# Performance work log

Measured on AMD Instinct MI355X. Metric: run time of the kernel, lower is better.

## Reference

```python
import jax, jax.numpy as jnp
import numpy as np

B, S, E, H = 4, 2048, 1024, 16
D = E // H  # head_dim


def setup_inputs() -> dict:
    key = jax.random.key(0)
    ks = jax.random.split(key, 6)
    x = jax.random.normal(ks[0], (B, S, E), dtype=jnp.float32)
    # causal mask: 1 where attention allowed (lower triangular)
    mask = jnp.tril(jnp.ones((S, S), dtype=bool))
    scale = 1.0 / jnp.sqrt(E).astype(jnp.float32)  # init scale for linears
    w_q = jax.random.normal(ks[1], (E, E), dtype=jnp.float32) * scale
    w_k = jax.random.normal(ks[2], (E, E), dtype=jnp.float32) * scale
    w_v = jax.random.normal(ks[3], (E, E), dtype=jnp.float32) * scale
    w_o = jax.random.normal(ks[4], (E, E), dtype=jnp.float32) * scale
    b_o = jnp.zeros((E,), dtype=jnp.float32)
    return {"x": x, "mask": mask, "w_q": w_q, "w_k": w_k, "w_v": w_v,
            "w_o": w_o, "b_o": b_o}


def reference(x, mask, w_q, w_k, w_v, w_o, b_o):
    # torch Linear: y = x @ W.T ; weights stored [out, in]
    q = jnp.einsum('bse,fe->bsf', x, w_q).reshape(B, S, H, D).transpose(0, 2, 1, 3)
    k = jnp.einsum('bse,fe->bsf', x, w_k).reshape(B, S, H, D).transpose(0, 2, 1, 3)
    v = jnp.einsum('bse,fe->bsf', x, w_v).reshape(B, S, H, D).transpose(0, 2, 1, 3)
    scale = D ** -0.5
    scores = jnp.einsum('bhqd,bhkd->bhqk', q, k) * scale  # [B,H,S,S]
    scores = jnp.where(mask, scores, -jnp.inf)
    attn = jax.nn.softmax(scores, axis=-1)
    out = jnp.einsum('bhqk,bhkd->bhqd', attn, v)  # [B,H,S,D]
    out = out.transpose(0, 2, 1, 3).reshape(B, S, E)
    return jnp.einsum('bse,fe->bsf', out, w_o) + b_o
```

## Files before the change

kernel.cpp:

```cpp
#include <hip/hip_runtime.h>
#include <stdint.h>

#define B_ 4
#define S_ 2048
#define E_ 1024
#define H_ 16
#define D_ 64
#define LSTR 72
#define PSTR 72

typedef __bf16 bf16x8 __attribute__((ext_vector_type(8)));
typedef float f32x4 __attribute__((ext_vector_type(4)));

__device__ __forceinline__ f32x4 mfma16(bf16x8 a, bf16x8 b, f32x4 c) {
    return __builtin_amdgcn_mfma_f32_16x16x32_bf16(a, b, c, 0, 0, 0);
}

__device__ __forceinline__ float expsm(float s) {
    const float x = __builtin_fmaf(s, 0.18033688f, -17.31234049f);
    float r;
    asm("v_exp_f32 %0, %1" : "=v"(r) : "v"(x));
    return r;
}

__device__ __forceinline__ bf16x8 cvt8(const float* p) {
    const f32x4 a = *(const f32x4*)p;
    const f32x4 b = *(const f32x4*)(p + 4);
    bf16x8 r;
    r[0] = (__bf16)a[0]; r[1] = (__bf16)a[1]; r[2] = (__bf16)a[2]; r[3] = (__bf16)a[3];
    r[4] = (__bf16)b[0]; r[5] = (__bf16)b[1]; r[6] = (__bf16)b[2]; r[7] = (__bf16)b[3];
    return r;
}

__global__ __launch_bounds__(256)
void cvt_x(const float* __restrict__ s, __bf16* __restrict__ d) {
    const size_t i = ((size_t)blockIdx.x * 256 + threadIdx.x) * 8;
    *(bf16x8*)(d + i) = cvt8(s + i);
}

__global__ __launch_bounds__(256)
void cvt_w4(const float* __restrict__ w0, const float* __restrict__ w1,
            const float* __restrict__ w2, const float* __restrict__ w3,
            __bf16* __restrict__ d) {
    const size_t i = ((size_t)blockIdx.x * 256 + threadIdx.x) * 8;
    const int sel = (int)(i >> 20);
    const size_t off = i & ((1u << 20) - 1);
    const float* s = (sel == 0) ? w0 : (sel == 1) ? w1 : (sel == 2) ? w2 : w3;
    *(bf16x8*)(d + i) = cvt8(s + off);
}

template <int MODE>
__global__ __launch_bounds__(256)
void gemm_bt(const __bf16* __restrict__ A, const __bf16* __restrict__ Wb,
             const float* __restrict__ bias, void* __restrict__ outv) {
    __shared__ __bf16 Al[128 * 32];
    __shared__ __bf16 Bl[128 * 32];
    const int t = threadIdx.x;
    const int lane = t & 63;
    const int wave = t >> 6;
    const int ln = lane & 15, quad = lane >> 4;
    const int m0 = blockIdx.x * 128;
    const int n0 = blockIdx.y * 128;
    const __bf16* W = Wb + (MODE == 0 ? (size_t)blockIdx.z * E_ * E_ : 0);

    const int srow = wave * 16 + (lane >> 2);
    const int scol = (lane & 3) * 8;

    f32x4 acc[4][4];
#pragma unroll
    for (int i = 0; i < 4; i++)
#pragma unroll
        for (int j = 0; j < 4; j++) acc[i][j] = (f32x4){0.f, 0.f, 0.f, 0.f};

    for (int k0 = 0; k0 < E_; k0 += 32) {
#pragma unroll
        for (int p = 0; p < 2; p++) {
            const __bf16* ga = A + (size_t)(m0 + p * 64 + srow) * E_ + k0 + scol;
            const __bf16* gb = W + (size_t)(n0 + p * 64 + srow) * E_ + k0 + scol;
            __builtin_amdgcn_global_load_lds(
                (const __attribute__((address_space(1))) void*)ga,
                (__attribute__((address_space(3))) void*)(Al + p * 2048 + wave * 512), 16, 0, 0);
            __builtin_amdgcn_global_load_lds(
                (const __attribute__((address_space(1))) void*)gb,
                (__attribute__((address_space(3))) void*)(Bl + p * 2048 + wave * 512), 16, 0, 0);
        }
        asm volatile("s_waitcnt vmcnt(0)" ::: "memory");
        __syncthreads();

        bf16x8 a[4], b[4];
#pragma unroll
        for (int i = 0; i < 4; i++)
            a[i] = *(const bf16x8*)(Al + ((wave >> 1) * 64 + i * 16 + ln) * 32 + quad * 8);
#pragma unroll
        for (int j = 0; j < 4; j++)
            b[j] = *(const bf16x8*)(Bl + ((wave & 1) * 64 + j * 16 + ln) * 32 + quad * 8);
#pragma unroll
        for (int i = 0; i < 4; i++)
#pragma unroll
            for (int j = 0; j < 4; j++)
                acc[i][j] = mfma16(a[i], b[j], acc[i][j]);
        __syncthreads();
    }

    const int wm = (wave >> 1) * 64, wn = (wave & 1) * 64;
#pragma unroll
    for (int i = 0; i < 4; i++) {
#pragma unroll
        for (int j = 0; j < 4; j++) {
            const int n = n0 + wn + j * 16 + ln;
            const float bv = (MODE == 1) ? bias[n] : 0.f;
#pragma unroll
            for (int r = 0; r < 4; r++) {
                const int m = m0 + wm + i * 16 + quad * 4 + r;
                const float v = acc[i][j][r] + bv;
                if (MODE == 0) {
                    const int bb = m >> 11, s = m & (S_ - 1);
                    const int h = n >> 6, d = n & 63;
                    ((__bf16*)outv)[(size_t)blockIdx.z * (B_ * H_ * S_ * D_) +
                                    (((size_t)(bb * H_ + h)) * S_ + s) * D_ + d] = (__bf16)v;
                } else {
                    ((float*)outv)[(size_t)m * E_ + n] = v;
                }
            }
        }
    }
}

template <typename TA, typename TO, bool STORE_BHSD>
__global__ __launch_bounds__(256)
void proj_fb(const TA* __restrict__ A, const float* __restrict__ W,
             const float* __restrict__ bias, TO* __restrict__ out) {
    const int lane = threadIdx.x & 63;
    const int wave = threadIdx.x >> 6;
    const int ln = lane & 15, quad = lane >> 4;
    const int m0 = blockIdx.x * 128 + (wave >> 1) * 64;
    const int n0 = blockIdx.y * 128 + (wave & 1) * 64;
    f32x4 acc[4][4];
#pragma unroll
    for (int i = 0; i < 4; i++)
#pragma unroll
        for (int j = 0; j < 4; j++) acc[i][j] = (f32x4){0.f, 0.f, 0.f, 0.f};
    for (int k0 = 0; k0 < E_; k0 += 32) {
        bf16x8 a[4], b[4];
#pragma unroll
        for (int i = 0; i < 4; i++) {
            const TA* p = A + (size_t)(m0 + i * 16 + ln) * E_ + k0 + quad * 8;
            if constexpr (sizeof(TA) == 4) a[i] = cvt8((const float*)p);
            else a[i] = *(const bf16x8*)p;
        }
#pragma unroll
        for (int j = 0; j < 4; j++)
            b[j] = cvt8(W + (size_t)(n0 + j * 16 + ln) * E_ + k0 + quad * 8);
#pragma unroll
        for (int i = 0; i < 4; i++)
#pragma unroll
            for (int j = 0; j < 4; j++) acc[i][j] = mfma16(a[i], b[j], acc[i][j]);
    }
#pragma unroll
    for (int i = 0; i < 4; i++)
#pragma unroll
        for (int j = 0; j < 4; j++) {
            const int n = n0 + j * 16 + ln;
            const float bv = bias ? bias[n] : 0.f;
#pragma unroll
            for (int r = 0; r < 4; r++) {
                const int m = m0 + i * 16 + quad * 4 + r;
                const float v = acc[i][j][r] + bv;
                if (STORE_BHSD) {
                    const int bb = m >> 11, s = m & (S_ - 1);
                    const int h = n >> 6, d = n & 63;
                    out[(((size_t)(bb * H_ + h)) * S_ + s) * D_ + d] = (TO)v;
                } else {
                    out[(size_t)m * E_ + n] = (TO)v;
                }
            }
        }
}

__global__ __launch_bounds__(512, 4)
void attn_kernel(const __bf16* __restrict__ Q, const __bf16* __restrict__ K,
                 const __bf16* __restrict__ V, __bf16* __restrict__ O) {
    __shared__ __align__(16) __bf16 Kl[2][64 * LSTR];
    __shared__ __align__(16) __bf16 Vt[2][64 * LSTR];
    __shared__ __align__(16) __bf16 Pl[8][16 * PSTR];

    const int t = threadIdx.x;
    const int lane = t & 63;
    const int wave = t >> 6;
    const int ln = lane & 15, quad = lane >> 4;
    const int bh = blockIdx.x & 63;
    const int pair = blockIdx.x >> 6;
    const int b = bh >> 4, h = bh & 15;
    const __bf16* Qh = Q + (size_t)bh * S_ * D_;
    const __bf16* Kh = K + (size_t)bh * S_ * D_;
    const __bf16* Vh = V + (size_t)bh * S_ * D_;

    const int krK = t >> 3, dcK = (t & 7) * 8;
    const int krV = t & 63, dcV = (t >> 6) * 8;

    __bf16* Pw = Pl[wave];
    bf16x8 ones;
#pragma unroll
    for (int j = 0; j < 8; j++) ones[j] = (__bf16)1.0f;

#pragma unroll 1
    for (int pass = 0; pass < 2; pass++) {
        const int qt = pass ? (15 - pair) : pair;
        const int q0 = qt * 128 + wave * 16;
        const int nkb = 2 * qt + 2;

        const bf16x8 aq0 = *(const bf16x8*)(Qh + (size_t)(q0 + ln) * D_ + quad * 8);
        const bf16x8 aq1 = *(const bf16x8*)(Qh + (size_t)(q0 + ln) * D_ + 32 + quad * 8);

        f32x4 o[4], lacc;
        lacc = (f32x4){0.f, 0.f, 0.f, 0.f};
#pragma unroll
        for (int nt = 0; nt < 4; nt++) o[nt] = (f32x4){0.f, 0.f, 0.f, 0.f};

        bf16x8 kv = *(const bf16x8*)(Kh + (size_t)krK * D_ + dcK);
        bf16x8 vv = *(const bf16x8*)(Vh + (size_t)krV * D_ + dcV);
        *(bf16x8*)(Kl[0] + krK * LSTR + dcK) = kv;
#pragma unroll
        for (int j = 0; j < 8; j++) Vt[0][(dcV + j) * LSTR + krV] = vv[j];
        kv = *(const bf16x8*)(Kh + (size_t)(64 + krK) * D_ + dcK);
        vv = *(const bf16x8*)(Vh + (size_t)(64 + krV) * D_ + dcV);
        __syncthreads();

#pragma unroll 1
        for (int kb = 0; kb < nkb; kb++) {
            const int k0 = kb * 64;
            const __bf16* Kc = Kl[kb & 1];
            const __bf16* Vc = Vt[kb & 1];

            f32x4 sacc[4];
#pragma unroll
            for (int nt = 0; nt < 4; nt++) sacc[nt] = (f32x4){0.f, 0.f, 0.f, 0.f};
            __builtin_amdgcn_s_setprio(1);
#pragma unroll
            for (int nt = 0; nt < 4; nt++) {
                bf16x8 bk0 = *(const bf16x8*)(Kc + (nt * 16 + ln) * LSTR + quad * 8);
                bf16x8 bk1 = *(const bf16x8*)(Kc + (nt * 16 + ln) * LSTR + 32 + quad * 8);
                sacc[nt] = mfma16(aq0, bk0, sacc[nt]);
                sacc[nt] = mfma16(aq1, bk1, sacc[nt]);
            }
            __builtin_amdgcn_s_setprio(0);

            if (k0 + 63 > q0) {
#pragma unroll
                for (int nt = 0; nt < 4; nt++) {
                    const int col = k0 + nt * 16 + ln;
#pragma unroll
                    for (int r = 0; r < 4; r++) {
                        const int row = q0 + quad * 4 + r;
                        const float p = (col <= row) ? expsm(sacc[nt][r]) : 0.f;
                        Pw[(quad * 4 + r) * PSTR + nt * 16 + ln] = (__bf16)p;
                    }
                }
            } else {
#pragma unroll
                for (int nt = 0; nt < 4; nt++)
#pragma unroll
                    for (int r = 0; r < 4; r++)
                        Pw[(quad * 4 + r) * PSTR + nt * 16 + ln] = (__bf16)expsm(sacc[nt][r]);
            }
            asm volatile("s_waitcnt lgkmcnt(0)" ::: "memory");

            const bf16x8 ap0 = *(const bf16x8*)(Pw + ln * PSTR + quad * 8);
            const bf16x8 ap1 = *(const bf16x8*)(Pw + ln * PSTR + 32 + quad * 8);

            __builtin_amdgcn_s_setprio(1);
#pragma unroll
            for (int nt = 0; nt < 4; nt++) {
                bf16x8 bv0 = *(const bf16x8*)(Vc + (nt * 16 + ln) * LSTR + quad * 8);
                bf16x8 bv1 = *(const bf16x8*)(Vc + (nt * 16 + ln) * LSTR + 32 + quad * 8);
                o[nt] = mfma16(ap0, bv0, o[nt]);
                o[nt] = mfma16(ap1, bv1, o[nt]);
            }
            lacc = mfma16(ap0, ones, lacc);
            lacc = mfma16(ap1, ones, lacc);
            __builtin_amdgcn_s_setprio(0);

            if (kb + 1 < nkb) {
                __bf16* Kn = Kl[(kb + 1) & 1];
                __bf16* Vn = Vt[(kb + 1) & 1];
                *(bf16x8*)(Kn + krK * LSTR + dcK) = kv;
#pragma unroll
                for (int j = 0; j < 8; j++) Vn[(dcV + j) * LSTR + krV] = vv[j];
                if (kb + 2 < nkb) {
                    const int kn = k0 + 128;
                    kv = *(const bf16x8*)(Kh + (size_t)(kn + krK) * D_ + dcK);
                    vv = *(const bf16x8*)(Vh + (size_t)(kn + krV) * D_ + dcV);
                }
            }
            __syncthreads();
        }

        float inv[4];
#pragma unroll
        for (int r = 0; r < 4; r++) inv[r] = 1.f / lacc[r];
#pragma unroll
        for (int nt = 0; nt < 4; nt++) {
#pragma unroll
            for (int r = 0; r < 4; r++) {
                const int s = q0 + quad * 4 + r;
                const int e = h * 64 + nt * 16 + ln;
                O[((size_t)b * S_ + s) * E_ + e] = (__bf16)(o[nt][r] * inv[r]);
            }
        }
    }
}

extern "C" void kernel_launch(void* const* d_in, const int* in_sizes, int n_in,
                              void* d_out, int out_size, void* d_ws, size_t ws_size,
                              hipStream_t stream) {
    const void* xv = nullptr;
    const void* wv[4] = {nullptr, nullptr, nullptr, nullptr};
    const void* bov = nullptr;
    int wn = 0;
    for (int i = 0; i < n_in; i++) {
        const int sz = in_sizes[i];
        if (sz == B_ * S_ * E_) xv = d_in[i];
        else if (sz == E_ * E_) { if (wn < 4) wv[wn++] = d_in[i]; }
        else if (sz == E_) bov = d_in[i];
    }
    if (!xv) xv = d_in[0];
    if (wn < 4) {
        int base = (n_in >= 7) ? 2 : 1;
        for (int j = 0; j < 4; j++) wv[j] = d_in[base + j];
        bov = d_in[base + 4];
    }
    const float* x = (const float*)xv;
    const float* b_o = (const float*)bov;
    float* out = (float*)d_out;

    char* ws = (char*)d_ws;
    const size_t MB = 1024 * 1024;
    const size_t need = 256 + 88 * MB;

    if (ws_size >= need) {
        __bf16* xb = (__bf16*)(ws + 256);
        __bf16* wb = (__bf16*)(ws + 256 + 16 * MB);
        __bf16* Qb = (__bf16*)(ws + 256 + 24 * MB);
        __bf16* Kb = (__bf16*)(ws + 256 + 40 * MB);
        __bf16* Vb = (__bf16*)(ws + 256 + 56 * MB);
        __bf16* Ob = (__bf16*)(ws + 256 + 72 * MB);

        cvt_x<<<4096, 256, 0, stream>>>(x, xb);
        cvt_w4<<<2048, 256, 0, stream>>>((const float*)wv[0], (const float*)wv[1],
                                         (const float*)wv[2], (const float*)wv[3], wb);

        gemm_bt<0><<<dim3(64, 8, 3), 256, 0, stream>>>(xb, wb, nullptr, Qb);
        attn_kernel<<<512, 512, 0, stream>>>(Qb, Kb, Vb, Ob);
        gemm_bt<1><<<dim3(64, 8), 256, 0, stream>>>(Ob, wb + (size_t)3 * E_ * E_, b_o, out);
    } else {
        const size_t buf = (size_t)B_ * H_ * S_ * D_ * sizeof(__bf16);
        __bf16* Qb = (__bf16*)(ws + 256);
        __bf16* Kb = (__bf16*)(ws + 256 + buf);
        __bf16* Vb = (__bf16*)(ws + 256 + 2 * buf);
        __bf16* Ob = (__bf16*)(ws + 256 + 3 * buf);
        const dim3 gproj(B_ * S_ / 128, E_ / 128);
        proj_fb<float, __bf16, true><<<gproj, 256, 0, stream>>>(x, (const float*)wv[0], nullptr, Qb);
        proj_fb<float, __bf16, true><<<gproj, 256, 0, stream>>>(x, (const float*)wv[1], nullptr, Kb);
        proj_fb<float, __bf16, true><<<gproj, 256, 0, stream>>>(x, (const float*)wv[2], nullptr, Vb);
        attn_kernel<<<512, 512, 0, stream>>>(Qb, Kb, Vb, Ob);
        proj_fb<__bf16, float, false><<<gproj, 256, 0, stream>>>(Ob, (const float*)wv[3], b_o, out);
    }
}
```

Measured before the change: 259.3 us.

## Swizzle K/V shared-memory layout, raise attention occupancy, merge conversion kernels

Replaces the padded K and transposed-V LDS tiles with an unpadded XOR-swizzled layout. This shrinks shared memory per block and is meant to avoid bank conflicts on the MFMA operand reads. Launch bounds for the attention kernel go from 4 to 6 waves per SIMD, which lets more blocks co-reside but may constrain registers and cause spills. The two fp32-to-bf16 conversion kernels are fused into one launch to save launch overhead.

```diff
diff --git a/kernel.cpp b/kernel.cpp
--- a/kernel.cpp
+++ b/kernel.cpp
@@ -6,8 +6,11 @@
 #define E_ 1024
 #define H_ 16
 #define D_ 64
-#define LSTR 72
 #define PSTR 72
+
+__device__ __forceinline__ int kvswz(int row, int col) {
+    return row * 64 + (col ^ ((row & 7) << 3));
+}
 
 typedef __bf16 bf16x8 __attribute__((ext_vector_type(8)));
 typedef float f32x4 __attribute__((ext_vector_type(4)));
@@ -33,20 +36,21 @@
 }
 
 __global__ __launch_bounds__(256)
-void cvt_x(const float* __restrict__ s, __bf16* __restrict__ d) {
-    const size_t i = ((size_t)blockIdx.x * 256 + threadIdx.x) * 8;
-    *(bf16x8*)(d + i) = cvt8(s + i);
-}
-
-__global__ __launch_bounds__(256)
-void cvt_w4(const float* __restrict__ w0, const float* __restrict__ w1,
-            const float* __restrict__ w2, const float* __restrict__ w3,
-            __bf16* __restrict__ d) {
-    const size_t i = ((size_t)blockIdx.x * 256 + threadIdx.x) * 8;
-    const int sel = (int)(i >> 20);
-    const size_t off = i & ((1u << 20) - 1);
-    const float* s = (sel == 0) ? w0 : (sel == 1) ? w1 : (sel == 2) ? w2 : w3;
-    *(bf16x8*)(d + i) = cvt8(s + off);
+void cvt_all(const float* __restrict__ x, const float* __restrict__ w0,
+             const float* __restrict__ w1, const float* __restrict__ w2,
+             const float* __restrict__ w3, __bf16* __restrict__ xb,
+             __bf16* __restrict__ wb) {
+    const size_t g = ((size_t)blockIdx.x * 256 + threadIdx.x) * 8;
+    const size_t NX = (size_t)B_ * S_ * E_;
+    if (g < NX) {
+        *(bf16x8*)(xb + g) = cvt8(x + g);
+    } else {
+        const size_t i = g - NX;
+        const int sel = (int)(i >> 20);
+        const size_t off = i & ((1u << 20) - 1);
+        const float* s = (sel == 0) ? w0 : (sel == 1) ? w1 : (sel == 2) ? w2 : w3;
+        *(bf16x8*)(wb + i) = cvt8(s + off);
+    }
 }
 
 template <int MODE>
@@ -177,11 +181,11 @@
         }
 }
 
-__global__ __launch_bounds__(512, 4)
+__global__ __launch_bounds__(512, 6)
 void attn_kernel(const __bf16* __restrict__ Q, const __bf16* __restrict__ K,
                  const __bf16* __restrict__ V, __bf16* __restrict__ O) {
-    __shared__ __align__(16) __bf16 Kl[2][64 * LSTR];
-    __shared__ __align__(16) __bf16 Vt[2][64 * LSTR];
+    __shared__ __align__(16) __bf16 Kl[2][64 * 64];
+    __shared__ __align__(16) __bf16 Vt[2][64 * 64];
     __shared__ __align__(16) __bf16 Pl[8][16 * PSTR];
 
     const int t = threadIdx.x;
@@ -219,9 +223,11 @@
 
         bf16x8 kv = *(const bf16x8*)(Kh + (size_t)krK * D_ + dcK);
         bf16x8 vv = *(const bf16x8*)(Vh + (size_t)krV * D_ + dcV);
-        *(bf16x8*)(Kl[0] + krK * LSTR + dcK) = kv;
-#pragma unroll
-        for (int j = 0; j < 8; j++) Vt[0][(dcV + j) * LSTR + krV] = vv[j];
+        *(bf16x8*)(Kl[0] + kvswz(krK, dcK)) = kv;
+#pragma unroll
+        for (int j = 0; j < 8; j++) {
+            Vt[0][kvswz(dcV + j, krV)] = vv[j];
+        }
         kv = *(const bf16x8*)(Kh + (size_t)(64 + krK) * D_ + dcK);
         vv = *(const bf16x8*)(Vh + (size_t)(64 + krV) * D_ + dcV);
         __syncthreads();
@@ -238,8 +244,9 @@
             __builtin_amdgcn_s_setprio(1);
 #pragma unroll
             for (int nt = 0; nt < 4; nt++) {
-                bf16x8 bk0 = *(const bf16x8*)(Kc + (nt * 16 + ln) * LSTR + quad * 8);
-                bf16x8 bk1 = *(const bf16x8*)(Kc + (nt * 16 + ln) * LSTR + 32 + quad * 8);
+                const int rk = nt * 16 + ln;
+                bf16x8 bk0 = *(const bf16x8*)(Kc + kvswz(rk, quad * 8));
+                bf16x8 bk1 = *(const bf16x8*)(Kc + kvswz(rk, 32 + quad * 8));
                 sacc[nt] = mfma16(aq0, bk0, sacc[nt]);
                 sacc[nt] = mfma16(aq1, bk1, sacc[nt]);
             }
@@ -271,8 +278,9 @@
             __builtin_amdgcn_s_setprio(1);
 #pragma unroll
             for (int nt = 0; nt < 4; nt++) {
-                bf16x8 bv0 = *(const bf16x8*)(Vc + (nt * 16 + ln) * LSTR + quad * 8);
-                bf16x8 bv1 = *(const bf16x8*)(Vc + (nt * 16 + ln) * LSTR + 32 + quad * 8);
+                const int rv = nt * 16 + ln;
+                bf16x8 bv0 = *(const bf16x8*)(Vc + kvswz(rv, quad * 8));
+                bf16x8 bv1 = *(const bf16x8*)(Vc + kvswz(rv, 32 + quad * 8));
                 o[nt] = mfma16(ap0, bv0, o[nt]);
                 o[nt] = mfma16(ap1, bv1, o[nt]);
             }
@@ -283,9 +291,11 @@
             if (kb + 1 < nkb) {
                 __bf16* Kn = Kl[(kb + 1) & 1];
                 __bf16* Vn = Vt[(kb + 1) & 1];
-                *(bf16x8*)(Kn + krK * LSTR + dcK) = kv;
-#pragma unroll
-                for (int j = 0; j < 8; j++) Vn[(dcV + j) * LSTR + krV] = vv[j];
+                *(bf16x8*)(Kn + kvswz(krK, dcK)) = kv;
+#pragma unroll
+                for (int j = 0; j < 8; j++) {
+                    Vn[kvswz(dcV + j, krV)] = vv[j];
+                }
                 if (kb + 2 < nkb) {
                     const int kn = k0 + 128;
                     kv = *(const bf16x8*)(Kh + (size_t)(kn + krK) * D_ + dcK);
@@ -345,9 +355,8 @@
         __bf16* Vb = (__bf16*)(ws + 256 + 56 * MB);
         __bf16* Ob = (__bf16*)(ws + 256 + 72 * MB);
 
-        cvt_x<<<4096, 256, 0, stream>>>(x, xb);
-        cvt_w4<<<2048, 256, 0, stream>>>((const float*)wv[0], (const float*)wv[1],
-                                         (const float*)wv[2], (const float*)wv[3], wb);
+        cvt_all<<<6144, 256, 0, stream>>>(x, (const float*)wv[0], (const float*)wv[1],
+                                          (const float*)wv[2], (const float*)wv[3], xb, wb);
 
         gemm_bt<0><<<dim3(64, 8, 3), 256, 0, stream>>>(xb, wb, nullptr, Qb);
         attn_kernel<<<512, 512, 0, stream>>>(Qb, Kb, Vb, Ob);
```

Measured after the change: 283.3 us. 1.09x slower.
